# Performance work log

Hardware: AMD Instinct MI355X
Metric: run time of the kernel (lower is better)

Reference implementation:

```python
import jax, jax.numpy as jnp
import numpy as np

N_EMBD = 384
NUM_HEADS = 6
HEAD_SIZE = 64
B, T = 64, 256


def setup_inputs() -> dict:
    key = jax.random.key(0)
    ks = jax.random.split(key, 6)
    s = 0.02
    x = jax.random.normal(ks[0], (B, T, N_EMBD), dtype=jnp.float32)
    # per-head projection weights, stored as [H, in, out] so y = x @ W
    Wq = jax.random.normal(ks[1], (NUM_HEADS, N_EMBD, HEAD_SIZE), dtype=jnp.float32) * s
    Wk = jax.random.normal(ks[2], (NUM_HEADS, N_EMBD, HEAD_SIZE), dtype=jnp.float32) * s
    Wv = jax.random.normal(ks[3], (NUM_HEADS, N_EMBD, HEAD_SIZE), dtype=jnp.float32) * s
    Wp = jax.random.normal(ks[4], (NUM_HEADS * HEAD_SIZE, N_EMBD), dtype=jnp.float32) * s
    bp = jax.random.normal(ks[5], (N_EMBD,), dtype=jnp.float32) * s
    return {"x": x, "Wq": Wq, "Wk": Wk, "Wv": Wv, "Wp": Wp, "bp": bp}


def reference(x, Wq, Wk, Wv, Wp, bp):
    # x: [B,T,C]; W{q,k,v}: [H,C,D]; dropout is identity (eval mode)
    Bb, Tt, _ = x.shape
    q = jnp.einsum('btc,hcd->bhtd', x, Wq)
    k = jnp.einsum('btc,hcd->bhtd', x, Wk)
    v = jnp.einsum('btc,hcd->bhtd', x, Wv)
    scale = HEAD_SIZE ** -0.5
    scores = jnp.einsum('bhtd,bhsd->bhts', q, k) * scale  # [B,H,T,T]
    causal = jnp.tril(jnp.ones((Tt, Tt), dtype=bool))
    scores = jnp.where(causal, scores, jnp.finfo(scores.dtype).min)
    attn = jax.nn.softmax(scores, axis=-1)
    out = jnp.einsum('bhts,bhsd->bhtd', attn, v)  # [B,H,T,D]
    out = out.transpose(0, 2, 1, 3).reshape(Bb, Tt, NUM_HEADS * HEAD_SIZE)
    return out @ Wp + bp
```

## Files before the change

### kernel.cpp

```cpp
#include <hip/hip_runtime.h>
#include <stdint.h>

#define B_  64
#define T_  256
#define C_  384
#define H_  6
#define D_  64
#define NTOK (B_*T_)

typedef float f32x4 __attribute__((ext_vector_type(4)));
typedef short s16x8 __attribute__((ext_vector_type(8)));

__device__ __forceinline__ unsigned short f2bf(float f) {
    unsigned int u;
    __builtin_memcpy(&u, &f, 4);
    u = u + 0x7FFFu + ((u >> 16) & 1u);
    return (unsigned short)(u >> 16);
}

__device__ __forceinline__ void async_copy16(const unsigned short* g, unsigned short* l) {
    __builtin_amdgcn_global_load_lds(
        (const __attribute__((address_space(1))) unsigned int*)g,
        (__attribute__((address_space(3))) unsigned int*)l, 16, 0, 0);
}

__global__ __launch_bounds__(256) void transpose_weights(
    const float* __restrict__ Wq, const float* __restrict__ Wk,
    const float* __restrict__ Wv, const float* __restrict__ Wp,
    unsigned short* __restrict__ W3, unsigned short* __restrict__ WTp) {
    __shared__ float tile[32][33];
    int z = blockIdx.y;
    const float* in;
    unsigned short* out;
    int R, Cc;
    if (z < 18) {
        int proj = z / 6, h = z % 6;
        const float* Wsrc = proj == 0 ? Wq : (proj == 1 ? Wk : Wv);
        in = Wsrc + h * C_ * D_;
        out = W3 + (size_t)(h * 192 + proj * 64) * C_;
        R = C_; Cc = D_;
    } else {
        in = Wp; out = WTp; R = C_; Cc = C_;
    }
    int tilesC = Cc / 32;
    int tilesR = R / 32;
    int bx = blockIdx.x;
    if (bx >= tilesC * tilesR) return;
    int tr = bx / tilesC, tc = bx % tilesC;
    int tx = threadIdx.x & 31;
    int ty8 = threadIdx.x >> 5;
    int gx = tc * 32 + tx;
#pragma unroll
    for (int i = 0; i < 4; i++) {
        int gy = tr * 32 + ty8 + i * 8;
        tile[ty8 + i * 8][tx] = in[gy * Cc + gx];
    }
    __syncthreads();
#pragma unroll
    for (int i = 0; i < 4; i++) {
        int oy = tc * 32 + ty8 + i * 8;
        int ox = tr * 32 + tx;
        out[oy * R + ox] = f2bf(tile[tx][ty8 + i * 8]);
    }
}

__global__ __launch_bounds__(512, 2) void fused_attn(
    const float* __restrict__ X, const unsigned short* __restrict__ W3,
    unsigned short* __restrict__ Ows) {
    __shared__ alignas(16) unsigned short smem[67584];
    unsigned short* Wc     = smem;
    unsigned short* q_lds  = smem + 18432;
    unsigned short* k_lds  = q_lds + 16384;
    unsigned short* vT_lds = k_lds + 16384;

    int bh = blockIdx.x;
    int h = bh >> 6, b = bh & 63;
    int tid = threadIdx.x;
    int w = tid >> 6, lane = tid & 63;
    int n16 = lane & 15, q4 = lane >> 4;
    const int jt[2] = {w, 15 - w};

    const unsigned short* W3h = W3 + (size_t)h * 192 * C_;
    const float* xb = X + (size_t)b * T_ * C_;

    f32x4 acc[2][12];
#pragma unroll
    for (int i = 0; i < 2; i++)
#pragma unroll
        for (int j = 0; j < 12; j++) acc[i][j] = (f32x4){0.f, 0.f, 0.f, 0.f};

    for (int kc = 0; kc < 4; kc++) {
        int ko = kc * 96;
        float4 a0[2][3], a1[2][3];
#pragma unroll
        for (int mi = 0; mi < 2; mi++)
#pragma unroll
            for (int ks = 0; ks < 3; ks++) {
                const float* ap = xb + (size_t)(jt[mi] * 16 + n16) * C_ + ko + ks * 32 + q4 * 8;
                a0[mi][ks] = *reinterpret_cast<const float4*>(ap);
                a1[mi][ks] = *reinterpret_cast<const float4*>(ap + 4);
            }
        if (kc) __syncthreads();
#pragma unroll
        for (int i = 0; i < 5; i++) {
            int sb = i * 512 + w * 64;
            if (sb < 2304) {
                int L = sb + lane;
                int row = L / 12;
                int c = L % 12;
                int ks = c >> 2;
                int q4g = (c & 3) ^ (row & 3);
                async_copy16(W3h + (size_t)row * C_ + ko + ks * 32 + q4g * 8,
                             Wc + (size_t)sb * 8);
            }
        }
        __syncthreads();
#pragma unroll
        for (int ks = 0; ks < 3; ks++) {
            s16x8 af[2];
#pragma unroll
            for (int mi = 0; mi < 2; mi++) {
                float4 lo = a0[mi][ks], hi = a1[mi][ks];
                s16x8 a;
                a[0] = (short)f2bf(lo.x); a[1] = (short)f2bf(lo.y);
                a[2] = (short)f2bf(lo.z); a[3] = (short)f2bf(lo.w);
                a[4] = (short)f2bf(hi.x); a[5] = (short)f2bf(hi.y);
                a[6] = (short)f2bf(hi.z); a[7] = (short)f2bf(hi.w);
                af[mi] = a;
            }
#pragma unroll
            for (int ni = 0; ni < 12; ni++) {
                int row = ni * 16 + n16;
                int cp = ks * 4 + (q4 ^ (row & 3));
                s16x8 bf = *reinterpret_cast<const s16x8*>(&Wc[row * 96 + cp * 8]);
                if (ni < 8) {
                    acc[0][ni] = __builtin_amdgcn_mfma_f32_16x16x32_bf16(bf, af[0], acc[0][ni], 0, 0, 0);
                    acc[1][ni] = __builtin_amdgcn_mfma_f32_16x16x32_bf16(bf, af[1], acc[1][ni], 0, 0, 0);
                } else {
                    acc[0][ni] = __builtin_amdgcn_mfma_f32_16x16x32_bf16(af[0], bf, acc[0][ni], 0, 0, 0);
                    acc[1][ni] = __builtin_amdgcn_mfma_f32_16x16x32_bf16(af[1], bf, acc[1][ni], 0, 0, 0);
                }
            }
        }
    }
#pragma unroll
    for (int mi = 0; mi < 2; mi++) {
        int tile = jt[mi];
#pragma unroll
        for (int ni = 0; ni < 12; ni++) {
            ushort4 pk;
            pk.x = f2bf(acc[mi][ni][0]); pk.y = f2bf(acc[mi][ni][1]);
            pk.z = f2bf(acc[mi][ni][2]); pk.w = f2bf(acc[mi][ni][3]);
            if (ni < 8) {
                int t = tile * 16 + n16;
                int cp = (2 * (ni & 3) + (q4 >> 1)) ^ (n16 & 7);
                unsigned short* dst = (ni < 4) ? q_lds : k_lds;
                *reinterpret_cast<ushort4*>(&dst[t * 64 + cp * 8 + (q4 & 1) * 4]) = pk;
            } else {
                int d = (ni - 8) * 16 + n16;
                int cp = (tile * 2 + (q4 >> 1)) ^ (d & 7);
                *reinterpret_cast<ushort4*>(&vT_lds[d * 256 + cp * 8 + (q4 & 1) * 4]) = pk;
            }
        }
    }
    __syncthreads();

    unsigned short* pw_base = smem + w * 1280;
    const f32x4 zero4 = (f32x4){0.f, 0.f, 0.f, 0.f};

#pragma unroll
    for (int tt = 0; tt < 2; tt++) {
        int j = jt[tt];
        int t0 = j * 16;
        int tq = t0 + n16;
        s16x8 qa0 = *reinterpret_cast<const s16x8*>(&q_lds[tq * 64 + ((q4 ^ (n16 & 7)) * 8)]);
        s16x8 qa1 = *reinterpret_cast<const s16x8*>(&q_lds[tq * 64 + (((q4 + 4) ^ (n16 & 7)) * 8)]);

        f32x4 o[4];
        float l_lane[4];
#pragma unroll
        for (int i = 0; i < 4; i++) o[i] = zero4;
#pragma unroll
        for (int r = 0; r < 4; r++) l_lane[r] = 0.f;

        int nch = j / 2 + 1;
        for (int c = 0; c < nch; c++) {
            int s0 = c * 32;
            bool bAct = (s0 + 16) < (t0 + 16);
            int r0 = s0 + n16, r1 = s0 + 16 + n16;
            s16x8 k00 = *reinterpret_cast<const s16x8*>(&k_lds[r0 * 64 + ((q4 ^ (r0 & 7)) * 8)]);
            s16x8 k01 = *reinterpret_cast<const s16x8*>(&k_lds[r0 * 64 + (((q4 + 4) ^ (r0 & 7)) * 8)]);
            f32x4 sv0 = __builtin_amdgcn_mfma_f32_16x16x32_bf16(qa0, k00, zero4, 0, 0, 0);
            sv0 = __builtin_amdgcn_mfma_f32_16x16x32_bf16(qa1, k01, sv0, 0, 0, 0);
            f32x4 sv1 = zero4;
            if (bAct) {
                s16x8 k10 = *reinterpret_cast<const s16x8*>(&k_lds[r1 * 64 + ((q4 ^ (r1 & 7)) * 8)]);
                s16x8 k11 = *reinterpret_cast<const s16x8*>(&k_lds[r1 * 64 + (((q4 + 4) ^ (r1 & 7)) * 8)]);
                sv1 = __builtin_amdgcn_mfma_f32_16x16x32_bf16(qa0, k10, zero4, 0, 0, 0);
                sv1 = __builtin_amdgcn_mfma_f32_16x16x32_bf16(qa1, k11, sv1, 0, 0, 0);
            }
            unsigned short* pw = pw_base + (c & 1) * 640;
#pragma unroll
            for (int r = 0; r < 4; r++) {
                int t = t0 + q4 * 4 + r;
                float pA = (s0 + n16 <= t) ? __expf(sv0[r] * 0.125f) : 0.f;
                float pB = (bAct && (s0 + 16 + n16 <= t)) ? __expf(sv1[r] * 0.125f) : 0.f;
                l_lane[r] += pA + pB;
                pw[(q4 * 4 + r) * 40 + n16] = f2bf(pA);
                pw[(q4 * 4 + r) * 40 + 16 + n16] = f2bf(pB);
            }
            s16x8 pa = *reinterpret_cast<const s16x8*>(&pw[n16 * 40 + q4 * 8]);
#pragma unroll
            for (int dt = 0; dt < 4; dt++) {
                int d = dt * 16 + n16;
                int jp = (c * 4 + q4) ^ (d & 7);
                s16x8 vf = *reinterpret_cast<const s16x8*>(&vT_lds[d * 256 + jp * 8]);
                o[dt] = __builtin_amdgcn_mfma_f32_16x16x32_bf16(pa, vf, o[dt], 0, 0, 0);
            }
        }

        float linv[4];
#pragma unroll
        for (int r = 0; r < 4; r++) {
            float l = l_lane[r];
            l += __shfl_xor(l, 1);
            l += __shfl_xor(l, 2);
            l += __shfl_xor(l, 4);
            l += __shfl_xor(l, 8);
            linv[r] = 1.0f / l;
        }
#pragma unroll
        for (int dt = 0; dt < 4; dt++) {
            int col = h * 64 + dt * 16 + n16;
#pragma unroll
            for (int r = 0; r < 4; r++)
                Ows[(size_t)(b * T_ + t0 + q4 * 4 + r) * C_ + col] = f2bf(o[dt][r] * linv[r]);
        }
    }
}

__global__ __launch_bounds__(256) void gemm_out(
    const unsigned short* __restrict__ A, const unsigned short* __restrict__ WTp,
    const float* __restrict__ bp, float* __restrict__ out) {
    __shared__ alignas(16) unsigned short Bt[6 * 128 * 32];
    int m0 = blockIdx.x * 128;
    int n0 = blockIdx.y * 128;
    int tid = threadIdx.x;
    int w = tid >> 6, lane = tid & 63;
    int n16 = lane & 15, q4 = lane >> 4;

    f32x4 acc[2][8];
#pragma unroll
    for (int i = 0; i < 2; i++)
#pragma unroll
        for (int j = 0; j < 8; j++) acc[i][j] = (f32x4){0.f, 0.f, 0.f, 0.f};

    const unsigned short* a_base[2];
#pragma unroll
    for (int mi = 0; mi < 2; mi++)
        a_base[mi] = A + (size_t)(m0 + w * 32 + mi * 16 + n16) * C_ + q4 * 8;

    for (int half = 0; half < 2; half++) {
        int ko = half * 192;
        s16x8 af[2][6];
#pragma unroll
        for (int mi = 0; mi < 2; mi++)
#pragma unroll
            for (int ks = 0; ks < 6; ks++)
                af[mi][ks] = *reinterpret_cast<const s16x8*>(a_base[mi] + ko + ks * 32);
        if (half) __syncthreads();
#pragma unroll
        for (int i = 0; i < 12; i++) {
            int L = w * 768 + i * 64 + lane;
            int kstep = L >> 9;
            int rem = L & 511;
            int row = rem >> 2;
            int j = (rem & 3) ^ (row & 3);
            async_copy16(WTp + (size_t)(n0 + row) * C_ + ko + kstep * 32 + j * 8,
                         Bt + (size_t)(w * 768 + i * 64) * 8);
        }
        __syncthreads();
#pragma unroll
        for (int ks = 0; ks < 6; ks++) {
            s16x8 bf[8];
#pragma unroll
            for (int ni = 0; ni < 8; ni++) {
                int row = ni * 16 + n16;
                int jp = q4 ^ (row & 3);
                bf[ni] = *reinterpret_cast<const s16x8*>(&Bt[ks * 4096 + row * 32 + jp * 8]);
            }
#pragma unroll
            for (int mi = 0; mi < 2; mi++)
#pragma unroll
                for (int ni = 0; ni < 8; ni++)
                    acc[mi][ni] = __builtin_amdgcn_mfma_f32_16x16x32_bf16(
                        bf[ni], af[mi][ks], acc[mi][ni], 0, 0, 0);
        }
    }

#pragma unroll
    for (int mi = 0; mi < 2; mi++) {
        int tr = m0 + w * 32 + mi * 16 + n16;
#pragma unroll
        for (int ni = 0; ni < 8; ni++) {
            int c0 = n0 + ni * 16 + q4 * 4;
            float4 bias = *reinterpret_cast<const float4*>(&bp[c0]);
            float4 res;
            res.x = acc[mi][ni][0] + bias.x;
            res.y = acc[mi][ni][1] + bias.y;
            res.z = acc[mi][ni][2] + bias.z;
            res.w = acc[mi][ni][3] + bias.w;
            *reinterpret_cast<float4*>(&out[(size_t)tr * C_ + c0]) = res;
        }
    }
}

extern "C" void kernel_launch(void* const* d_in, const int* in_sizes, int n_in,
                              void* d_out, int out_size, void* d_ws, size_t ws_size,
                              hipStream_t stream) {
    const float* x  = (const float*)d_in[0];
    const float* Wq = (const float*)d_in[1];
    const float* Wk = (const float*)d_in[2];
    const float* Wv = (const float*)d_in[3];
    const float* Wp = (const float*)d_in[4];
    const float* bp = (const float*)d_in[5];
    float* out = (float*)d_out;

    char* ws = (char*)d_ws;
    size_t off = 0;
    auto alloc = [&](size_t bytes) -> unsigned short* {
        unsigned short* p = (unsigned short*)(ws + off);
        off += (bytes + 255) & ~(size_t)255;
        return p;
    };
    unsigned short* W3  = alloc((size_t)H_ * 192 * C_ * 2);
    unsigned short* WTp = alloc((size_t)C_ * C_ * 2);
    unsigned short* Ows = alloc((size_t)NTOK * C_ * 2);

    transpose_weights<<<dim3(144, 19), dim3(256), 0, stream>>>(
        Wq, Wk, Wv, Wp, W3, WTp);
    fused_attn<<<dim3(B_ * H_), dim3(512), 0, stream>>>(x, W3, Ows);
    gemm_out<<<dim3(128, 3), dim3(256), 0, stream>>>(Ows, WTp, bp, out);
}
```

Before: 151.3 us.

## Shrink LDS footprint by aliasing Q/K/V over weight buffer, raise occupancy

```diff
diff --git a/kernel.cpp b/kernel.cpp
--- a/kernel.cpp
+++ b/kernel.cpp
@@ -64,14 +64,14 @@
     }
 }
 
-__global__ __launch_bounds__(512, 2) void fused_attn(
+__global__ __launch_bounds__(512, 4) void fused_attn(
     const float* __restrict__ X, const unsigned short* __restrict__ W3,
     unsigned short* __restrict__ Ows) {
-    __shared__ alignas(16) unsigned short smem[67584];
-    unsigned short* Wc     = smem;
-    unsigned short* q_lds  = smem + 18432;
-    unsigned short* k_lds  = q_lds + 16384;
-    unsigned short* vT_lds = k_lds + 16384;
+    __shared__ alignas(16) unsigned short smem[37888];
+    unsigned short* region = smem;
+    unsigned short* k_lds  = region;
+    unsigned short* vT_lds = region + 16384;
+    unsigned short* p_scr  = smem + 32768;
 
     int bh = blockIdx.x;
     int h = bh >> 6, b = bh & 63;
@@ -111,7 +111,7 @@
                 int ks = c >> 2;
                 int q4g = (c & 3) ^ (row & 3);
                 async_copy16(W3h + (size_t)row * C_ + ko + ks * 32 + q4g * 8,
-                             Wc + (size_t)sb * 8);
+                             region + (size_t)sb * 8);
             }
         }
         __syncthreads();
@@ -132,7 +132,7 @@
             for (int ni = 0; ni < 12; ni++) {
                 int row = ni * 16 + n16;
                 int cp = ks * 4 + (q4 ^ (row & 3));
-                s16x8 bf = *reinterpret_cast<const s16x8*>(&Wc[row * 96 + cp * 8]);
+                s16x8 bf = *reinterpret_cast<const s16x8*>(&region[row * 96 + cp * 8]);
                 if (ni < 8) {
                     acc[0][ni] = __builtin_amdgcn_mfma_f32_16x16x32_bf16(bf, af[0], acc[0][ni], 0, 0, 0);
                     acc[1][ni] = __builtin_amdgcn_mfma_f32_16x16x32_bf16(bf, af[1], acc[1][ni], 0, 0, 0);
@@ -143,19 +143,41 @@
             }
         }
     }
+    __syncthreads();
+
+#pragma unroll
+    for (int mi = 0; mi < 2; mi++) {
+        int t = jt[mi] * 16 + n16;
+#pragma unroll
+        for (int ni = 0; ni < 4; ni++) {
+            ushort4 pk;
+            pk.x = f2bf(acc[mi][ni][0]); pk.y = f2bf(acc[mi][ni][1]);
+            pk.z = f2bf(acc[mi][ni][2]); pk.w = f2bf(acc[mi][ni][3]);
+            int cp = (2 * (ni & 3) + (q4 >> 1)) ^ (n16 & 7);
+            *reinterpret_cast<ushort4*>(&region[t * 64 + cp * 8 + (q4 & 1) * 4]) = pk;
+        }
+    }
+    s16x8 qa[2][2];
+#pragma unroll
+    for (int mi = 0; mi < 2; mi++) {
+        int t = jt[mi] * 16 + n16;
+        qa[mi][0] = *reinterpret_cast<const s16x8*>(&region[t * 64 + ((q4 ^ (n16 & 7)) * 8)]);
+        qa[mi][1] = *reinterpret_cast<const s16x8*>(&region[t * 64 + (((q4 + 4) ^ (n16 & 7)) * 8)]);
+    }
+    __syncthreads();
+
 #pragma unroll
     for (int mi = 0; mi < 2; mi++) {
         int tile = jt[mi];
 #pragma unroll
-        for (int ni = 0; ni < 12; ni++) {
+        for (int ni = 4; ni < 12; ni++) {
             ushort4 pk;
             pk.x = f2bf(acc[mi][ni][0]); pk.y = f2bf(acc[mi][ni][1]);
             pk.z = f2bf(acc[mi][ni][2]); pk.w = f2bf(acc[mi][ni][3]);
             if (ni < 8) {
                 int t = tile * 16 + n16;
                 int cp = (2 * (ni & 3) + (q4 >> 1)) ^ (n16 & 7);
-                unsigned short* dst = (ni < 4) ? q_lds : k_lds;
-                *reinterpret_cast<ushort4*>(&dst[t * 64 + cp * 8 + (q4 & 1) * 4]) = pk;
+                *reinterpret_cast<ushort4*>(&k_lds[t * 64 + cp * 8 + (q4 & 1) * 4]) = pk;
             } else {
                 int d = (ni - 8) * 16 + n16;
                 int cp = (tile * 2 + (q4 >> 1)) ^ (d & 7);
@@ -165,16 +187,15 @@
     }
     __syncthreads();
 
-    unsigned short* pw_base = smem + w * 1280;
+    unsigned short* pw = p_scr + w * 640;
     const f32x4 zero4 = (f32x4){0.f, 0.f, 0.f, 0.f};
 
 #pragma unroll
     for (int tt = 0; tt < 2; tt++) {
         int j = jt[tt];
         int t0 = j * 16;
-        int tq = t0 + n16;
-        s16x8 qa0 = *reinterpret_cast<const s16x8*>(&q_lds[tq * 64 + ((q4 ^ (n16 & 7)) * 8)]);
-        s16x8 qa1 = *reinterpret_cast<const s16x8*>(&q_lds[tq * 64 + (((q4 + 4) ^ (n16 & 7)) * 8)]);
+        s16x8 qa0 = qa[tt][0];
+        s16x8 qa1 = qa[tt][1];
 
         f32x4 o[4];
         float l_lane[4];
@@ -199,7 +220,6 @@
                 sv1 = __builtin_amdgcn_mfma_f32_16x16x32_bf16(qa0, k10, zero4, 0, 0, 0);
                 sv1 = __builtin_amdgcn_mfma_f32_16x16x32_bf16(qa1, k11, sv1, 0, 0, 0);
             }
-            unsigned short* pw = pw_base + (c & 1) * 640;
 #pragma unroll
             for (int r = 0; r < 4; r++) {
                 int t = t0 + q4 * 4 + r;
```

Result: slower. 212.3 us (+40.4%).
